# Optimization experiments

Hardware: AMD Instinct MI355X
Metric: run time of the kernel (lower is better)

The kernel has to match this reference:

```python
import jax, jax.numpy as jnp
import numpy as np

N = 50000      # nodes
E = 600000     # edges
G = 512        # graphs in batch
F_IN = 128     # input node features
H = 128        # hidden size (both layers)
PH = 128       # pool/classifier hidden size


def setup_inputs() -> dict:
    key = jax.random.key(0)
    ks = jax.random.split(key, 12)
    def lin(k, fi, fo):
        return (jax.random.normal(k, (fi, fo), jnp.float32) / np.sqrt(fi)).astype(jnp.float32)
    return {
        "x": jax.random.normal(ks[0], (N, F_IN), jnp.float32),
        "edge_index": jax.random.randint(ks[1], (2, E), 0, N),
        "batch": jnp.sort(jax.random.randint(ks[2], (N,), 0, G)),
        "W1": lin(ks[3], F_IN, H), "b1": jnp.zeros((H,), jnp.float32),
        "ln1_g": jnp.ones((H,), jnp.float32), "ln1_b": jnp.zeros((H,), jnp.float32),
        "W2": lin(ks[4], H, H), "b2": jnp.zeros((H,), jnp.float32),
        "ln2_g": jnp.ones((H,), jnp.float32), "ln2_b": jnp.zeros((H,), jnp.float32),
        "gate_w1": lin(ks[5], H, PH), "gate_b1": jnp.zeros((PH,), jnp.float32),
        "gate_w2": lin(ks[6], PH, 1), "gate_b2": jnp.zeros((1,), jnp.float32),
        "cls_w1": lin(ks[7], H, PH), "cls_b1": jnp.zeros((PH,), jnp.float32),
        "cls_w2": lin(ks[8], PH, 2), "cls_b2": jnp.zeros((2,), jnp.float32),
    }


def _layer_norm(h, g, b):
    m = h.mean(-1, keepdims=True)
    v = ((h - m) ** 2).mean(-1, keepdims=True)
    return (h - m) * jax.lax.rsqrt(v + 1e-5) * g + b


def _gcn(x, src, dst, norm, W, b):
    # GCNConv: x' = D^{-1/2} (A+I) D^{-1/2} (x W) + b
    h = x @ W
    out = jax.ops.segment_sum(h[src] * norm[:, None], dst, num_segments=N)
    return out + b


def reference(x, edge_index, batch, W1, b1, ln1_g, ln1_b, W2, b2, ln2_g, ln2_b,
              gate_w1, gate_b1, gate_w2, gate_b2, cls_w1, cls_b1, cls_w2, cls_b2):
    loops = jnp.arange(N, dtype=edge_index.dtype)
    src = jnp.concatenate([edge_index[0], loops])
    dst = jnp.concatenate([edge_index[1], loops])
    deg = jax.ops.segment_sum(jnp.ones_like(src, dtype=x.dtype), dst, num_segments=N)
    dinv = jnp.where(deg > 0, jax.lax.rsqrt(jnp.maximum(deg, 1e-12)), 0.0)
    norm = dinv[src] * dinv[dst]  # [(E+N)]

    h = jax.nn.relu(_layer_norm(_gcn(x, src, dst, norm, W1, b1), ln1_g, ln1_b))
    h = jax.nn.relu(_layer_norm(_gcn(h, src, dst, norm, W2, b2), ln2_g, ln2_b))

    # GlobalAttention pooling: gate MLP -> scatter softmax over graphs -> weighted sum
    gate = (jax.nn.relu(h @ gate_w1 + gate_b1) @ gate_w2 + gate_b2)[:, 0]  # [N]
    gmax = jax.ops.segment_max(gate, batch, num_segments=G)
    a = jnp.exp(gate - gmax[batch])
    denom = jax.ops.segment_sum(a, batch, num_segments=G)
    alpha = a / denom[batch]
    pooled = jax.ops.segment_sum(alpha[:, None] * h, batch, num_segments=G)  # [G, H]

    logits = jax.nn.relu(pooled @ cls_w1 + cls_b1) @ cls_w2 + cls_b2  # [G, 2]
    return logits
```

## Files before the change

kernel.cpp:

```cpp
#include <hip/hip_runtime.h>
#include <hip/hip_bf16.h>

typedef short s8v __attribute__((ext_vector_type(8)));
typedef float f4v __attribute__((ext_vector_type(4)));

__device__ __forceinline__ unsigned short f2bf(float f) {
  unsigned int u = __builtin_bit_cast(unsigned int, f);
  unsigned int r = u + 0x7fffu + ((u >> 16) & 1u);
  return (unsigned short)(r >> 16);
}
__device__ __forceinline__ float bf2f(unsigned short s) {
  return __builtin_bit_cast(float, ((unsigned int)s) << 16);
}
__device__ __forceinline__ float bflo(unsigned int v) {
  return __builtin_bit_cast(float, (unsigned int)(v << 16));
}
__device__ __forceinline__ float bfhi(unsigned int v) {
  return __builtin_bit_cast(float, (unsigned int)(v & 0xffff0000u));
}
__device__ __forceinline__ unsigned int packbf(float a, float b) {
  return (unsigned int)f2bf(a) | ((unsigned int)f2bf(b) << 16);
}

__device__ __forceinline__ int lower_bound_i(const int* a, int n, int key) {
  int lo = 0, hi = n;
  while (lo < hi) { int mid = (lo + hi) >> 1; if (a[mid] < key) lo = mid + 1; else hi = mid; }
  return lo;
}

__global__ void accum_deg(const int* __restrict__ dst, unsigned int* __restrict__ deg, int E) {
  int e = blockIdx.x * blockDim.x + threadIdx.x;
  if (e < E) atomicAdd(&deg[dst[e]], 1u);
}

__global__ __launch_bounds__(256) void scanA(const unsigned int* __restrict__ deg,
                                             int* __restrict__ offs, int* __restrict__ partial,
                                             float* __restrict__ dinv, int n) {
  __shared__ int sh[256];
  int t = threadIdx.x;
  int i = blockIdx.x * 256 + t;
  int v = (i < n) ? (int)deg[i] : 0;
  if (i < n) dinv[i] = rsqrtf((float)(deg[i] + 1u));
  sh[t] = v;
  __syncthreads();
  for (int o = 1; o < 256; o <<= 1) {
    int add = (t >= o) ? sh[t - o] : 0;
    __syncthreads();
    sh[t] += add;
    __syncthreads();
  }
  if (i < n) offs[i] = sh[t] - v;
  if (t == 255) partial[blockIdx.x] = sh[255];
}

__global__ __launch_bounds__(256) void scanC(int* __restrict__ offs, const int* __restrict__ partial,
                                             int* __restrict__ cursor, int n, int E) {
  __shared__ int red[256];
  int bid = blockIdx.x;
  int t = threadIdx.x;
  int s = 0;
  for (int j = t; j < bid; j += 256) s += partial[j];
  red[t] = s;
  __syncthreads();
#pragma unroll
  for (int o = 128; o > 0; o >>= 1) {
    if (t < o) red[t] += red[t + o];
    __syncthreads();
  }
  int pre = red[0];
  int i = bid * 256 + t;
  if (i < n) {
    int o = offs[i] + pre;
    offs[i] = o;
    cursor[i] = o;
  }
  if (i == 0) offs[n] = E;
}

__global__ __launch_bounds__(256) void scatter_csr(const int* __restrict__ src, const int* __restrict__ dst,
                                                   int* __restrict__ cursor, int* __restrict__ col, int E) {
  int e = blockIdx.x * 256 + threadIdx.x;
  if (e < E) {
    int slot = atomicAdd(&cursor[dst[e]], 1);
    col[slot] = src[e];
  }
}

__global__ __launch_bounds__(256) void pack_w3(const float* __restrict__ Wa, const float* __restrict__ Wb,
                                               const float* __restrict__ Wc, unsigned short* __restrict__ P) {
  int gidx = blockIdx.x * 256 + threadIdx.x;
  if (gidx >= 3 * 32768) return;
  int which = gidx >> 15;
  int idx = gidx & 32767;
  const float* W = (which == 0) ? Wa : (which == 1) ? Wb : Wc;
  int j = idx & 15;
  int lane = (idx >> 4) & 63;
  int t = (idx >> 10) & 7;
  int c = (idx >> 13) & 3;
  int k = c * 32 + (lane >> 4) * 8 + (j & 7);
  int n = t * 16 + (lane & 15);
  float f = W[k * 128 + n];
  unsigned short hi = f2bf(f);
  unsigned short outv = (j < 8) ? hi : f2bf(f - bf2f(hi));
  P[gidx] = outv;
}

__global__ __launch_bounds__(256) void gemm_f32in(
    const float* __restrict__ in, const unsigned short* __restrict__ P,
    unsigned short* __restrict__ out, int n) {
  __shared__ unsigned short wlds[32768];
  int tid = threadIdx.x;
  for (int i = tid; i < 4096; i += 256)
    reinterpret_cast<uint4*>(wlds)[i] = reinterpret_cast<const uint4*>(P)[i];
  __syncthreads();

  int wave = tid >> 6, lane = tid & 63;
  int quad = lane >> 4, col = lane & 15;
  int base = blockIdx.x * 64 + wave * 16;
  int m = base + col;

  f4v acc[8];
#pragma unroll
  for (int t = 0; t < 8; ++t) acc[t] = (f4v){0.f, 0.f, 0.f, 0.f};

  for (int c = 0; c < 4; ++c) {
    s8v ah, al;
    float v[8];
    if (m < n) {
      const float4* xp = reinterpret_cast<const float4*>(in + (size_t)m * 128 + c * 32 + quad * 8);
      float4 v0 = xp[0], v1 = xp[1];
      v[0] = v0.x; v[1] = v0.y; v[2] = v0.z; v[3] = v0.w;
      v[4] = v1.x; v[5] = v1.y; v[6] = v1.z; v[7] = v1.w;
    } else {
#pragma unroll
      for (int j = 0; j < 8; ++j) v[j] = 0.f;
    }
#pragma unroll
    for (int j = 0; j < 8; ++j) {
      unsigned short h = f2bf(v[j]);
      ah[j] = (short)h;
      al[j] = (short)f2bf(v[j] - bf2f(h));
    }
#pragma unroll
    for (int t = 0; t < 8; ++t) {
      const s8v* bp = reinterpret_cast<const s8v*>(&wlds[((c * 8 + t) * 64 + lane) * 16]);
      s8v bh = bp[0], bl = bp[1];
      acc[t] = __builtin_amdgcn_mfma_f32_16x16x32_bf16(ah, bh, acc[t], 0, 0, 0);
      acc[t] = __builtin_amdgcn_mfma_f32_16x16x32_bf16(ah, bl, acc[t], 0, 0, 0);
      acc[t] = __builtin_amdgcn_mfma_f32_16x16x32_bf16(al, bh, acc[t], 0, 0, 0);
    }
  }
#pragma unroll
  for (int t = 0; t < 8; ++t)
#pragma unroll
    for (int r = 0; r < 4; ++r) {
      int mm = base + quad * 4 + r;
      if (mm < n) out[(size_t)mm * 128 + t * 16 + col] = f2bf(acc[t][r]);
    }
}

__global__ __launch_bounds__(256) void gemm_b16in(
    const unsigned short* __restrict__ in, const unsigned short* __restrict__ P,
    unsigned short* __restrict__ out, int n) {
  __shared__ unsigned short wlds[32768];
  int tid = threadIdx.x;
  for (int i = tid; i < 4096; i += 256)
    reinterpret_cast<uint4*>(wlds)[i] = reinterpret_cast<const uint4*>(P)[i];
  __syncthreads();

  int wave = tid >> 6, lane = tid & 63;
  int quad = lane >> 4, col = lane & 15;
  int base = blockIdx.x * 64 + wave * 16;
  int m = base + col;

  f4v acc[8];
#pragma unroll
  for (int t = 0; t < 8; ++t) acc[t] = (f4v){0.f, 0.f, 0.f, 0.f};

  for (int c = 0; c < 4; ++c) {
    s8v ah;
    if (m < n)
      ah = *reinterpret_cast<const s8v*>(in + (size_t)m * 128 + c * 32 + quad * 8);
    else
      ah = (s8v){0, 0, 0, 0, 0, 0, 0, 0};
#pragma unroll
    for (int t = 0; t < 8; ++t) {
      const s8v* bp = reinterpret_cast<const s8v*>(&wlds[((c * 8 + t) * 64 + lane) * 16]);
      s8v bh = bp[0], bl = bp[1];
      acc[t] = __builtin_amdgcn_mfma_f32_16x16x32_bf16(ah, bh, acc[t], 0, 0, 0);
      acc[t] = __builtin_amdgcn_mfma_f32_16x16x32_bf16(ah, bl, acc[t], 0, 0, 0);
    }
  }
#pragma unroll
  for (int t = 0; t < 8; ++t)
#pragma unroll
    for (int r = 0; r < 4; ++r) {
      int mm = base + quad * 4 + r;
      if (mm < n) out[(size_t)mm * 128 + t * 16 + col] = f2bf(acc[t][r]);
    }
}

__global__ __launch_bounds__(256) void gemm_gate(
    const unsigned short* __restrict__ in, const unsigned short* __restrict__ P,
    const float* __restrict__ gb1, const float* __restrict__ gw2,
    const float* __restrict__ gb2, float* __restrict__ gate, int n) {
  __shared__ unsigned short wlds[32768];
  int tid = threadIdx.x;
  for (int i = tid; i < 4096; i += 256)
    reinterpret_cast<uint4*>(wlds)[i] = reinterpret_cast<const uint4*>(P)[i];
  __syncthreads();

  int wave = tid >> 6, lane = tid & 63;
  int quad = lane >> 4, col = lane & 15;
  int base = blockIdx.x * 64 + wave * 16;
  int m = base + col;

  f4v acc[8];
#pragma unroll
  for (int t = 0; t < 8; ++t) acc[t] = (f4v){0.f, 0.f, 0.f, 0.f};

  for (int c = 0; c < 4; ++c) {
    s8v ah;
    if (m < n)
      ah = *reinterpret_cast<const s8v*>(in + (size_t)m * 128 + c * 32 + quad * 8);
    else
      ah = (s8v){0, 0, 0, 0, 0, 0, 0, 0};
#pragma unroll
    for (int t = 0; t < 8; ++t) {
      const s8v* bp = reinterpret_cast<const s8v*>(&wlds[((c * 8 + t) * 64 + lane) * 16]);
      s8v bh = bp[0], bl = bp[1];
      acc[t] = __builtin_amdgcn_mfma_f32_16x16x32_bf16(ah, bh, acc[t], 0, 0, 0);
      acc[t] = __builtin_amdgcn_mfma_f32_16x16x32_bf16(ah, bl, acc[t], 0, 0, 0);
    }
  }
  float bv[8], g2[8];
#pragma unroll
  for (int t = 0; t < 8; ++t) {
    bv[t] = gb1[t * 16 + col];
    g2[t] = gw2[t * 16 + col];
  }
  float gb2v = gb2[0];
#pragma unroll
  for (int r = 0; r < 4; ++r) {
    float p = 0.f;
#pragma unroll
    for (int t = 0; t < 8; ++t)
      p += fmaxf(acc[t][r] + bv[t], 0.f) * g2[t];
#pragma unroll
    for (int o = 1; o < 16; o <<= 1) p += __shfl_xor(p, o);
    int mm = base + quad * 4 + r;
    if (col == 0 && mm < n) gate[mm] = p + gb2v;
  }
}

__global__ __launch_bounds__(256) void gather_ln(
    const int* __restrict__ offs, const int* __restrict__ col,
    const float* __restrict__ dinv, const unsigned short* __restrict__ h,
    const float* __restrict__ bias, const float* __restrict__ gam,
    const float* __restrict__ bet, unsigned short* __restrict__ out, int n) {
  int wid = (int)((blockIdx.x * 256u + threadIdx.x) >> 6);
  int lane = threadIdx.x & 63;
  int grp = lane >> 4;
  int sub = lane & 15;
  int i = wid * 4 + grp;
  if (i >= n) return;
  const uint4* hu = reinterpret_cast<const uint4*>(h);
  float di = dinv[i];
  float sl = di * di;
  uint4 hv = hu[(size_t)i * 16 + sub];
  float4 b0v = reinterpret_cast<const float4*>(bias)[sub * 2];
  float4 b1v = reinterpret_cast<const float4*>(bias)[sub * 2 + 1];
  float v[8];
  v[0] = bflo(hv.x) * sl + b0v.x; v[1] = bfhi(hv.x) * sl + b0v.y;
  v[2] = bflo(hv.y) * sl + b0v.z; v[3] = bfhi(hv.y) * sl + b0v.w;
  v[4] = bflo(hv.z) * sl + b1v.x; v[5] = bfhi(hv.z) * sl + b1v.y;
  v[6] = bflo(hv.w) * sl + b1v.z; v[7] = bfhi(hv.w) * sl + b1v.w;
  int b0 = offs[i], b1 = offs[i + 1];
  int e = b0;
  for (; e + 4 <= b1; e += 4) {
    int s0 = col[e], s1 = col[e + 1], s2 = col[e + 2], s3 = col[e + 3];
    uint4 h0 = hu[(size_t)s0 * 16 + sub];
    uint4 h1 = hu[(size_t)s1 * 16 + sub];
    uint4 h2 = hu[(size_t)s2 * 16 + sub];
    uint4 h3 = hu[(size_t)s3 * 16 + sub];
    float n0 = dinv[s0] * di, n1 = dinv[s1] * di, n2 = dinv[s2] * di, n3 = dinv[s3] * di;
    v[0] += bflo(h0.x) * n0 + bflo(h1.x) * n1 + bflo(h2.x) * n2 + bflo(h3.x) * n3;
    v[1] += bfhi(h0.x) * n0 + bfhi(h1.x) * n1 + bfhi(h2.x) * n2 + bfhi(h3.x) * n3;
    v[2] += bflo(h0.y) * n0 + bflo(h1.y) * n1 + bflo(h2.y) * n2 + bflo(h3.y) * n3;
    v[3] += bfhi(h0.y) * n0 + bfhi(h1.y) * n1 + bfhi(h2.y) * n2 + bfhi(h3.y) * n3;
    v[4] += bflo(h0.z) * n0 + bflo(h1.z) * n1 + bflo(h2.z) * n2 + bflo(h3.z) * n3;
    v[5] += bfhi(h0.z) * n0 + bfhi(h1.z) * n1 + bfhi(h2.z) * n2 + bfhi(h3.z) * n3;
    v[6] += bflo(h0.w) * n0 + bflo(h1.w) * n1 + bflo(h2.w) * n2 + bflo(h3.w) * n3;
    v[7] += bfhi(h0.w) * n0 + bfhi(h1.w) * n1 + bfhi(h2.w) * n2 + bfhi(h3.w) * n3;
  }
  for (; e + 2 <= b1; e += 2) {
    int s0 = col[e], s1 = col[e + 1];
    uint4 h0 = hu[(size_t)s0 * 16 + sub];
    uint4 h1 = hu[(size_t)s1 * 16 + sub];
    float n0 = dinv[s0] * di, n1 = dinv[s1] * di;
    v[0] += bflo(h0.x) * n0 + bflo(h1.x) * n1;
    v[1] += bfhi(h0.x) * n0 + bfhi(h1.x) * n1;
    v[2] += bflo(h0.y) * n0 + bflo(h1.y) * n1;
    v[3] += bfhi(h0.y) * n0 + bfhi(h1.y) * n1;
    v[4] += bflo(h0.z) * n0 + bflo(h1.z) * n1;
    v[5] += bfhi(h0.z) * n0 + bfhi(h1.z) * n1;
    v[6] += bflo(h0.w) * n0 + bflo(h1.w) * n1;
    v[7] += bfhi(h0.w) * n0 + bfhi(h1.w) * n1;
  }
  if (e < b1) {
    int s0 = col[e];
    uint4 h0 = hu[(size_t)s0 * 16 + sub];
    float n0 = dinv[s0] * di;
    v[0] += bflo(h0.x) * n0; v[1] += bfhi(h0.x) * n0;
    v[2] += bflo(h0.y) * n0; v[3] += bfhi(h0.y) * n0;
    v[4] += bflo(h0.z) * n0; v[5] += bfhi(h0.z) * n0;
    v[6] += bflo(h0.w) * n0; v[7] += bfhi(h0.w) * n0;
  }
  float s = 0.f, q = 0.f;
#pragma unroll
  for (int j = 0; j < 8; ++j) { s += v[j]; q += v[j] * v[j]; }
#pragma unroll
  for (int o = 1; o < 16; o <<= 1) {
    s += __shfl_xor(s, o);
    q += __shfl_xor(q, o);
  }
  float m = s * (1.0f / 128.0f);
  float var = q * (1.0f / 128.0f) - m * m;
  float rs = rsqrtf(var + 1e-5f);
  float4 g0 = reinterpret_cast<const float4*>(gam)[sub * 2];
  float4 g1 = reinterpret_cast<const float4*>(gam)[sub * 2 + 1];
  float4 e0 = reinterpret_cast<const float4*>(bet)[sub * 2];
  float4 e1 = reinterpret_cast<const float4*>(bet)[sub * 2 + 1];
  uint4 ov;
  ov.x = packbf(fmaxf((v[0] - m) * rs * g0.x + e0.x, 0.f), fmaxf((v[1] - m) * rs * g0.y + e0.y, 0.f));
  ov.y = packbf(fmaxf((v[2] - m) * rs * g0.z + e0.z, 0.f), fmaxf((v[3] - m) * rs * g0.w + e0.w, 0.f));
  ov.z = packbf(fmaxf((v[4] - m) * rs * g1.x + e1.x, 0.f), fmaxf((v[5] - m) * rs * g1.y + e1.y, 0.f));
  ov.w = packbf(fmaxf((v[6] - m) * rs * g1.z + e1.z, 0.f), fmaxf((v[7] - m) * rs * g1.w + e1.w, 0.f));
  reinterpret_cast<uint4*>(out)[(size_t)i * 16 + sub] = ov;
}

__global__ __launch_bounds__(256) void pool_kernel(
    float* __restrict__ gate, const unsigned short* __restrict__ h,
    const int* __restrict__ batch, float* __restrict__ pooled, int n) {
  int g = blockIdx.x;
  int tid = threadIdx.x;
  __shared__ float red[256];
  __shared__ float red2[256];
  int lo = lower_bound_i(batch, n, g);
  int hi = lower_bound_i(batch, n, g + 1);
  if (lo >= hi) {
    if (tid < 128) pooled[(size_t)g * 128 + tid] = 0.0f;
    return;
  }
  float m = -3.0e38f;
  for (int i = lo + tid; i < hi; i += 256) m = fmaxf(m, gate[i]);
  red[tid] = m;
  __syncthreads();
#pragma unroll
  for (int o = 128; o > 0; o >>= 1) {
    if (tid < o) red[tid] = fmaxf(red[tid], red[tid + o]);
    __syncthreads();
  }
  m = red[0];
  __syncthreads();
  float s = 0.0f;
  for (int i = lo + tid; i < hi; i += 256) {
    float e = __expf(gate[i] - m);
    gate[i] = e;
    s += e;
  }
  red[tid] = s;
  __syncthreads();
#pragma unroll
  for (int o = 128; o > 0; o >>= 1) {
    if (tid < o) red[tid] += red[tid + o];
    __syncthreads();
  }
  float inv = 1.0f / red[0];
  __syncthreads();
  const unsigned int* hu = reinterpret_cast<const unsigned int*>(h);
  int j = tid & 63, rgp = tid >> 6;
  float a0 = 0.f, a1 = 0.f;
  int i = lo + rgp;
  for (; i + 4 < hi; i += 8) {
    unsigned int p0 = hu[(size_t)i * 64 + j];
    unsigned int p1 = hu[(size_t)(i + 4) * 64 + j];
    float w0 = gate[i], w1 = gate[i + 4];
    a0 += bflo(p0) * w0 + bflo(p1) * w1;
    a1 += bfhi(p0) * w0 + bfhi(p1) * w1;
  }
  if (i < hi) {
    unsigned int p0 = hu[(size_t)i * 64 + j];
    float w0 = gate[i];
    a0 += bflo(p0) * w0;
    a1 += bfhi(p0) * w0;
  }
  red[tid] = a0;
  red2[tid] = a1;
  __syncthreads();
  if (tid < 64) {
    float f0 = (red[tid] + red[tid + 64] + red[tid + 128] + red[tid + 192]) * inv;
    float f1 = (red2[tid] + red2[tid + 64] + red2[tid + 128] + red2[tid + 192]) * inv;
    reinterpret_cast<float2*>(pooled + (size_t)g * 128)[tid] = make_float2(f0, f1);
  }
}

__global__ __launch_bounds__(128) void classifier(
    const float* __restrict__ pooled, const float* __restrict__ w1,
    const float* __restrict__ b1, const float* __restrict__ w2,
    const float* __restrict__ b2, float* __restrict__ out) {
  int g = blockIdx.x, j = threadIdx.x;
  __shared__ float p[128];
  __shared__ float r[128];
  p[j] = pooled[(size_t)g * 128 + j];
  __syncthreads();
  float acc = 0.0f;
#pragma unroll 8
  for (int k = 0; k < 128; ++k) acc = fmaf(p[k], w1[k * 128 + j], acc);
  acc += b1[j];
  r[j] = fmaxf(acc, 0.0f);
  __syncthreads();
  if (j < 2) {
    float a = 0.0f;
    for (int k = 0; k < 128; ++k) a = fmaf(r[k], w2[k * 2 + j], a);
    out[g * 2 + j] = a + b2[j];
  }
}

static inline size_t alup(size_t x) { return (x + 255) & ~(size_t)255; }

extern "C" void kernel_launch(void* const* d_in, const int* in_sizes, int n_in,
                              void* d_out, int out_size, void* d_ws, size_t ws_size,
                              hipStream_t stream) {
  const float* x    = (const float*)d_in[0];
  const int*   ei   = (const int*)d_in[1];
  const int*   bat  = (const int*)d_in[2];
  const float* W1   = (const float*)d_in[3];
  const float* b1   = (const float*)d_in[4];
  const float* ln1g = (const float*)d_in[5];
  const float* ln1b = (const float*)d_in[6];
  const float* W2   = (const float*)d_in[7];
  const float* b2   = (const float*)d_in[8];
  const float* ln2g = (const float*)d_in[9];
  const float* ln2b = (const float*)d_in[10];
  const float* gw1  = (const float*)d_in[11];
  const float* gb1  = (const float*)d_in[12];
  const float* gw2  = (const float*)d_in[13];
  const float* gb2  = (const float*)d_in[14];
  const float* cw1  = (const float*)d_in[15];
  const float* cb1  = (const float*)d_in[16];
  const float* cw2  = (const float*)d_in[17];
  const float* cb2  = (const float*)d_in[18];

  const int N = in_sizes[2];
  const int E = in_sizes[1] / 2;
  const int G = out_size / 2;
  const int* src = ei;
  const int* dst = ei + E;

  int nb256 = (N + 255) / 256;
  int eb256 = (E + 255) / 256;
  int mfmaB = (N + 63) / 64;
  int gatherB = (N + 15) / 16;

  char* base = (char*)d_ws;
  unsigned int* deg = (unsigned int*)base; base += alup((size_t)N * 4);
  float* dinv = (float*)base;              base += alup((size_t)N * 4);
  int* offs = (int*)base;                  base += alup((size_t)(N + 1) * 4);
  int* cursor = (int*)base;                base += alup((size_t)N * 4);
  int* partial = (int*)base;               base += alup((size_t)nb256 * 4);
  int* col = (int*)base;                   base += alup((size_t)E * 4);
  unsigned short* pW = (unsigned short*)base; base += alup((size_t)3 * 32768 * 2);
  unsigned short* hbuf = (unsigned short*)base; base += alup((size_t)N * 128 * 2);
  unsigned short* hout = (unsigned short*)base; base += alup((size_t)N * 128 * 2);
  float* gate = (float*)base;              base += alup((size_t)N * 4);
  float* pooled = (float*)base;            base += alup((size_t)G * 128 * 4);

  unsigned short* pW1 = pW;
  unsigned short* pW2 = pW + 32768;
  unsigned short* pG1 = pW + 65536;

  float* out = (float*)d_out;

  hipMemsetAsync(deg, 0, (size_t)N * 4, stream);
  accum_deg<<<eb256, 256, 0, stream>>>(dst, deg, E);
  scanA<<<nb256, 256, 0, stream>>>(deg, offs, partial, dinv, N);
  scanC<<<nb256, 256, 0, stream>>>(offs, partial, cursor, N, E);
  scatter_csr<<<eb256, 256, 0, stream>>>(src, dst, cursor, col, E);
  pack_w3<<<384, 256, 0, stream>>>(W1, W2, gw1, pW);

  gemm_f32in<<<mfmaB, 256, 0, stream>>>(x, pW1, hbuf, N);
  gather_ln<<<gatherB, 256, 0, stream>>>(offs, col, dinv, hbuf, b1, ln1g, ln1b, hout, N);

  gemm_b16in<<<mfmaB, 256, 0, stream>>>(hout, pW2, hbuf, N);
  gather_ln<<<gatherB, 256, 0, stream>>>(offs, col, dinv, hbuf, b2, ln2g, ln2b, hout, N);

  gemm_gate<<<mfmaB, 256, 0, stream>>>(hout, pG1, gb1, gw2, gb2, gate, N);

  pool_kernel<<<G, 256, 0, stream>>>(gate, hout, bat, pooled, N);

  classifier<<<G, 128, 0, stream>>>(pooled, cw1, cb1, cw2, cb2, out);
}
```

Before: 289.7 us.

## Fuse launches: pack+zero, gemm1+CSR scatter, pool+classifier; store dinv with edge indices

Several small kernels are merged to cut launch count. The weight packing and degree zeroing become one kernel. The CSR scatter runs as extra blocks of the first GEMM launch. Pooling and the classifier become one kernel, which removes the pooled buffer. The CSR column array now stores each source's dinv next to its index, so the gather avoids a dependent dinv load, at the cost of twice the column-array bandwidth. The scatter and GEMM blocks in one grid also contend for occupancy, since every block reserves the 64KB LDS even when it only scatters.

```diff
diff --git a/kernel.cpp b/kernel.cpp
--- a/kernel.cpp
+++ b/kernel.cpp
@@ -26,6 +26,31 @@
   int lo = 0, hi = n;
   while (lo < hi) { int mid = (lo + hi) >> 1; if (a[mid] < key) lo = mid + 1; else hi = mid; }
   return lo;
+}
+
+__global__ __launch_bounds__(256) void pack_zero(
+    const float* __restrict__ Wa, const float* __restrict__ Wb, const float* __restrict__ Wc,
+    unsigned short* __restrict__ P, unsigned int* __restrict__ deg, int n) {
+  int bid = blockIdx.x;
+  if (bid >= 384) {
+    int i = (bid - 384) * 256 + threadIdx.x;
+    if (i < n) deg[i] = 0u;
+    return;
+  }
+  int gidx = bid * 256 + threadIdx.x;
+  int which = gidx >> 15;
+  int idx = gidx & 32767;
+  const float* W = (which == 0) ? Wa : (which == 1) ? Wb : Wc;
+  int j = idx & 15;
+  int lane = (idx >> 4) & 63;
+  int t = (idx >> 10) & 7;
+  int c = (idx >> 13) & 3;
+  int k = c * 32 + (lane >> 4) * 8 + (j & 7);
+  int nn = t * 16 + (lane & 15);
+  float f = W[k * 128 + nn];
+  unsigned short hi = f2bf(f);
+  unsigned short outv = (j < 8) ? hi : f2bf(f - bf2f(hi));
+  P[gidx] = outv;
 }
 
 __global__ void accum_deg(const int* __restrict__ dst, unsigned int* __restrict__ deg, int E) {
@@ -77,38 +102,23 @@
   if (i == 0) offs[n] = E;
 }
 
-__global__ __launch_bounds__(256) void scatter_csr(const int* __restrict__ src, const int* __restrict__ dst,
-                                                   int* __restrict__ cursor, int* __restrict__ col, int E) {
-  int e = blockIdx.x * 256 + threadIdx.x;
-  if (e < E) {
-    int slot = atomicAdd(&cursor[dst[e]], 1);
-    col[slot] = src[e];
-  }
-}
-
-__global__ __launch_bounds__(256) void pack_w3(const float* __restrict__ Wa, const float* __restrict__ Wb,
-                                               const float* __restrict__ Wc, unsigned short* __restrict__ P) {
-  int gidx = blockIdx.x * 256 + threadIdx.x;
-  if (gidx >= 3 * 32768) return;
-  int which = gidx >> 15;
-  int idx = gidx & 32767;
-  const float* W = (which == 0) ? Wa : (which == 1) ? Wb : Wc;
-  int j = idx & 15;
-  int lane = (idx >> 4) & 63;
-  int t = (idx >> 10) & 7;
-  int c = (idx >> 13) & 3;
-  int k = c * 32 + (lane >> 4) * 8 + (j & 7);
-  int n = t * 16 + (lane & 15);
-  float f = W[k * 128 + n];
-  unsigned short hi = f2bf(f);
-  unsigned short outv = (j < 8) ? hi : f2bf(f - bf2f(hi));
-  P[gidx] = outv;
-}
-
-__global__ __launch_bounds__(256) void gemm_f32in(
+__global__ __launch_bounds__(256) void gemm1_scatter(
     const float* __restrict__ in, const unsigned short* __restrict__ P,
-    unsigned short* __restrict__ out, int n) {
+    unsigned short* __restrict__ out, int n,
+    const int* __restrict__ src, const int* __restrict__ dst,
+    int* __restrict__ cursor, int2* __restrict__ col2,
+    const float* __restrict__ dinv, int E, int gemmBlocks) {
   __shared__ unsigned short wlds[32768];
+  if ((int)blockIdx.x >= gemmBlocks) {
+    int e = ((int)blockIdx.x - gemmBlocks) * 256 + threadIdx.x;
+    if (e < E) {
+      int d = dst[e];
+      int s = src[e];
+      int slot = atomicAdd(&cursor[d], 1);
+      col2[slot] = make_int2(s, __builtin_bit_cast(int, dinv[s]));
+    }
+    return;
+  }
   int tid = threadIdx.x;
   for (int i = tid; i < 4096; i += 256)
     reinterpret_cast<uint4*>(wlds)[i] = reinterpret_cast<const uint4*>(P)[i];
@@ -254,7 +264,7 @@
 }
 
 __global__ __launch_bounds__(256) void gather_ln(
-    const int* __restrict__ offs, const int* __restrict__ col,
+    const int* __restrict__ offs, const int2* __restrict__ col2,
     const float* __restrict__ dinv, const unsigned short* __restrict__ h,
     const float* __restrict__ bias, const float* __restrict__ gam,
     const float* __restrict__ bet, unsigned short* __restrict__ out, int n) {
@@ -278,12 +288,15 @@
   int b0 = offs[i], b1 = offs[i + 1];
   int e = b0;
   for (; e + 4 <= b1; e += 4) {
-    int s0 = col[e], s1 = col[e + 1], s2 = col[e + 2], s3 = col[e + 3];
-    uint4 h0 = hu[(size_t)s0 * 16 + sub];
-    uint4 h1 = hu[(size_t)s1 * 16 + sub];
-    uint4 h2 = hu[(size_t)s2 * 16 + sub];
-    uint4 h3 = hu[(size_t)s3 * 16 + sub];
-    float n0 = dinv[s0] * di, n1 = dinv[s1] * di, n2 = dinv[s2] * di, n3 = dinv[s3] * di;
+    int2 c0 = col2[e], c1 = col2[e + 1], c2 = col2[e + 2], c3 = col2[e + 3];
+    uint4 h0 = hu[(size_t)c0.x * 16 + sub];
+    uint4 h1 = hu[(size_t)c1.x * 16 + sub];
+    uint4 h2 = hu[(size_t)c2.x * 16 + sub];
+    uint4 h3 = hu[(size_t)c3.x * 16 + sub];
+    float n0 = __builtin_bit_cast(float, c0.y) * di;
+    float n1 = __builtin_bit_cast(float, c1.y) * di;
+    float n2 = __builtin_bit_cast(float, c2.y) * di;
+    float n3 = __builtin_bit_cast(float, c3.y) * di;
     v[0] += bflo(h0.x) * n0 + bflo(h1.x) * n1 + bflo(h2.x) * n2 + bflo(h3.x) * n3;
     v[1] += bfhi(h0.x) * n0 + bfhi(h1.x) * n1 + bfhi(h2.x) * n2 + bfhi(h3.x) * n3;
     v[2] += bflo(h0.y) * n0 + bflo(h1.y) * n1 + bflo(h2.y) * n2 + bflo(h3.y) * n3;
@@ -293,24 +306,10 @@
     v[6] += bflo(h0.w) * n0 + bflo(h1.w) * n1 + bflo(h2.w) * n2 + bflo(h3.w) * n3;
     v[7] += bfhi(h0.w) * n0 + bfhi(h1.w) * n1 + bfhi(h2.w) * n2 + bfhi(h3.w) * n3;
   }
-  for (; e + 2 <= b1; e += 2) {
-    int s0 = col[e], s1 = col[e + 1];
-    uint4 h0 = hu[(size_t)s0 * 16 + sub];
-    uint4 h1 = hu[(size_t)s1 * 16 + sub];
-    float n0 = dinv[s0] * di, n1 = dinv[s1] * di;
-    v[0] += bflo(h0.x) * n0 + bflo(h1.x) * n1;
-    v[1] += bfhi(h0.x) * n0 + bfhi(h1.x) * n1;
-    v[2] += bflo(h0.y) * n0 + bflo(h1.y) * n1;
-    v[3] += bfhi(h0.y) * n0 + bfhi(h1.y) * n1;
-    v[4] += bflo(h0.z) * n0 + bflo(h1.z) * n1;
-    v[5] += bfhi(h0.z) * n0 + bfhi(h1.z) * n1;
-    v[6] += bflo(h0.w) * n0 + bflo(h1.w) * n1;
-    v[7] += bfhi(h0.w) * n0 + bfhi(h1.w) * n1;
-  }
-  if (e < b1) {
-    int s0 = col[e];
-    uint4 h0 = hu[(size_t)s0 * 16 + sub];
-    float n0 = dinv[s0] * di;
+  for (; e < b1; ++e) {
+    int2 c0 = col2[e];
+    uint4 h0 = hu[(size_t)c0.x * 16 + sub];
+    float n0 = __builtin_bit_cast(float, c0.y) * di;
     v[0] += bflo(h0.x) * n0; v[1] += bfhi(h0.x) * n0;
     v[2] += bflo(h0.y) * n0; v[3] += bfhi(h0.y) * n0;
     v[4] += bflo(h0.z) * n0; v[5] += bfhi(h0.z) * n0;
@@ -339,91 +338,88 @@
   reinterpret_cast<uint4*>(out)[(size_t)i * 16 + sub] = ov;
 }
 
-__global__ __launch_bounds__(256) void pool_kernel(
+__global__ __launch_bounds__(256) void pool_cls(
     float* __restrict__ gate, const unsigned short* __restrict__ h,
-    const int* __restrict__ batch, float* __restrict__ pooled, int n) {
+    const int* __restrict__ batch,
+    const float* __restrict__ w1, const float* __restrict__ b1,
+    const float* __restrict__ w2, const float* __restrict__ b2,
+    float* __restrict__ out, int n) {
   int g = blockIdx.x;
   int tid = threadIdx.x;
   __shared__ float red[256];
   __shared__ float red2[256];
+  __shared__ float p[128];
+  __shared__ float r[128];
   int lo = lower_bound_i(batch, n, g);
   int hi = lower_bound_i(batch, n, g + 1);
   if (lo >= hi) {
-    if (tid < 128) pooled[(size_t)g * 128 + tid] = 0.0f;
-    return;
-  }
-  float m = -3.0e38f;
-  for (int i = lo + tid; i < hi; i += 256) m = fmaxf(m, gate[i]);
-  red[tid] = m;
-  __syncthreads();
-#pragma unroll
-  for (int o = 128; o > 0; o >>= 1) {
-    if (tid < o) red[tid] = fmaxf(red[tid], red[tid + o]);
-    __syncthreads();
-  }
-  m = red[0];
-  __syncthreads();
-  float s = 0.0f;
-  for (int i = lo + tid; i < hi; i += 256) {
-    float e = __expf(gate[i] - m);
-    gate[i] = e;
-    s += e;
-  }
-  red[tid] = s;
-  __syncthreads();
-#pragma unroll
-  for (int o = 128; o > 0; o >>= 1) {
-    if (tid < o) red[tid] += red[tid + o];
-    __syncthreads();
-  }
-  float inv = 1.0f / red[0];
-  __syncthreads();
-  const unsigned int* hu = reinterpret_cast<const unsigned int*>(h);
-  int j = tid & 63, rgp = tid >> 6;
-  float a0 = 0.f, a1 = 0.f;
-  int i = lo + rgp;
-  for (; i + 4 < hi; i += 8) {
-    unsigned int p0 = hu[(size_t)i * 64 + j];
-    unsigned int p1 = hu[(size_t)(i + 4) * 64 + j];
-    float w0 = gate[i], w1 = gate[i + 4];
-    a0 += bflo(p0) * w0 + bflo(p1) * w1;
-    a1 += bfhi(p0) * w0 + bfhi(p1) * w1;
-  }
-  if (i < hi) {
-    unsigned int p0 = hu[(size_t)i * 64 + j];
-    float w0 = gate[i];
-    a0 += bflo(p0) * w0;
-    a1 += bfhi(p0) * w0;
-  }
-  red[tid] = a0;
-  red2[tid] = a1;
-  __syncthreads();
-  if (tid < 64) {
-    float f0 = (red[tid] + red[tid + 64] + red[tid + 128] + red[tid + 192]) * inv;
-    float f1 = (red2[tid] + red2[tid + 64] + red2[tid + 128] + red2[tid + 192]) * inv;
-    reinterpret_cast<float2*>(pooled + (size_t)g * 128)[tid] = make_float2(f0, f1);
-  }
-}
-
-__global__ __launch_bounds__(128) void classifier(
-    const float* __restrict__ pooled, const float* __restrict__ w1,
-    const float* __restrict__ b1, const float* __restrict__ w2,
-    const float* __restrict__ b2, float* __restrict__ out) {
-  int g = blockIdx.x, j = threadIdx.x;
-  __shared__ float p[128];
-  __shared__ float r[128];
-  p[j] = pooled[(size_t)g * 128 + j];
-  __syncthreads();
+    if (tid < 128) p[tid] = 0.0f;
+  } else {
+    float m = -3.0e38f;
+    for (int i = lo + tid; i < hi; i += 256) m = fmaxf(m, gate[i]);
+    red[tid] = m;
+    __syncthreads();
+#pragma unroll
+    for (int o = 128; o > 0; o >>= 1) {
+      if (tid < o) red[tid] = fmaxf(red[tid], red[tid + o]);
+      __syncthreads();
+    }
+    m = red[0];
+    __syncthreads();
+    float s = 0.0f;
+    for (int i = lo + tid; i < hi; i += 256) {
+      float e = __expf(gate[i] - m);
+      gate[i] = e;
+      s += e;
+    }
+    red[tid] = s;
+    __syncthreads();
+#pragma unroll
+    for (int o = 128; o > 0; o >>= 1) {
+      if (tid < o) red[tid] += red[tid + o];
+      __syncthreads();
+    }
+    float inv = 1.0f / red[0];
+    __syncthreads();
+    const unsigned int* hu = reinterpret_cast<const unsigned int*>(h);
+    int j = tid & 63, rgp = tid >> 6;
+    float a0 = 0.f, a1 = 0.f;
+    int i = lo + rgp;
+    for (; i + 4 < hi; i += 8) {
+      unsigned int p0 = hu[(size_t)i * 64 + j];
+      unsigned int p1 = hu[(size_t)(i + 4) * 64 + j];
+      float w0 = gate[i], w1v = gate[i + 4];
+      a0 += bflo(p0) * w0 + bflo(p1) * w1v;
+      a1 += bfhi(p0) * w0 + bfhi(p1) * w1v;
+    }
+    if (i < hi) {
+      unsigned int p0 = hu[(size_t)i * 64 + j];
+      float w0 = gate[i];
+      a0 += bflo(p0) * w0;
+      a1 += bfhi(p0) * w0;
+    }
+    red[tid] = a0;
+    red2[tid] = a1;
+    __syncthreads();
+    if (tid < 64) {
+      p[2 * tid]     = (red[tid] + red[tid + 64] + red[tid + 128] + red[tid + 192]) * inv;
+      p[2 * tid + 1] = (red2[tid] + red2[tid + 64] + red2[tid + 128] + red2[tid + 192]) * inv;
+    }
+  }
+  __syncthreads();
+  int j = tid & 127, half = tid >> 7;
   float acc = 0.0f;
 #pragma unroll 8
-  for (int k = 0; k < 128; ++k) acc = fmaf(p[k], w1[k * 128 + j], acc);
-  acc += b1[j];
-  r[j] = fmaxf(acc, 0.0f);
-  __syncthreads();
-  if (j < 2) {
+  for (int k = half * 64; k < half * 64 + 64; ++k)
+    acc = fmaf(p[k], w1[k * 128 + j], acc);
+  red[tid] = acc;
+  __syncthreads();
+  if (tid < 128) r[tid] = fmaxf(red[tid] + red[tid + 128] + b1[tid], 0.0f);
+  __syncthreads();
+  if (tid < 2) {
     float a = 0.0f;
-    for (int k = 0; k < 128; ++k) a = fmaf(r[k], w2[k * 2 + j], a);
-    out[g * 2 + j] = a + b2[j];
+    for (int k = 0; k < 128; ++k) a = fmaf(r[k], w2[k * 2 + tid], a);
+    out[g * 2 + tid] = a + b2[tid];
   }
 }
 
@@ -469,12 +465,11 @@
   int* offs = (int*)base;                  base += alup((size_t)(N + 1) * 4);
   int* cursor = (int*)base;                base += alup((size_t)N * 4);
   int* partial = (int*)base;               base += alup((size_t)nb256 * 4);
-  int* col = (int*)base;                   base += alup((size_t)E * 4);
+  int2* col2 = (int2*)base;                base += alup((size_t)E * 8);
   unsigned short* pW = (unsigned short*)base; base += alup((size_t)3 * 32768 * 2);
   unsigned short* hbuf = (unsigned short*)base; base += alup((size_t)N * 128 * 2);
   unsigned short* hout = (unsigned short*)base; base += alup((size_t)N * 128 * 2);
   float* gate = (float*)base;              base += alup((size_t)N * 4);
-  float* pooled = (float*)base;            base += alup((size_t)G * 128 * 4);
 
   unsigned short* pW1 = pW;
   unsigned short* pW2 = pW + 32768;
@@ -482,22 +477,15 @@
 
   float* out = (float*)d_out;
 
-  hipMemsetAsync(deg, 0, (size_t)N * 4, stream);
+  pack_zero<<<384 + nb256, 256, 0, stream>>>(W1, W2, gw1, pW, deg, N);
   accum_deg<<<eb256, 256, 0, stream>>>(dst, deg, E);
   scanA<<<nb256, 256, 0, stream>>>(deg, offs, partial, dinv, N);
   scanC<<<nb256, 256, 0, stream>>>(offs, partial, cursor, N, E);
-  scatter_csr<<<eb256, 256, 0, stream>>>(src, dst, cursor, col, E);
-  pack_w3<<<384, 256, 0, stream>>>(W1, W2, gw1, pW);
-
-  gemm_f32in<<<mfmaB, 256, 0, stream>>>(x, pW1, hbuf, N);
-  gather_ln<<<gatherB, 256, 0, stream>>>(offs, col, dinv, hbuf, b1, ln1g, ln1b, hout, N);
-
+  gemm1_scatter<<<mfmaB + eb256, 256, 0, stream>>>(x, pW1, hbuf, N,
+                                                   src, dst, cursor, col2, dinv, E, mfmaB);
+  gather_ln<<<gatherB, 256, 0, stream>>>(offs, col2, dinv, hbuf, b1, ln1g, ln1b, hout, N);
   gemm_b16in<<<mfmaB, 256, 0, stream>>>(hout, pW2, hbuf, N);
-  gather_ln<<<gatherB, 256, 0, stream>>>(offs, col, dinv, hbuf, b2, ln2g, ln2b, hout, N);
-
+  gather_ln<<<gatherB, 256, 0, stream>>>(offs, col2, dinv, hbuf, b2, ln2g, ln2b, hout, N);
   gemm_gate<<<mfmaB, 256, 0, stream>>>(hout, pG1, gb1, gw2, gb2, gate, N);
-
-  pool_kernel<<<G, 256, 0, stream>>>(gate, hout, bat, pooled, N);
-
-  classifier<<<G, 128, 0, stream>>>(pooled, cw1, cb1, cw2, cb2, out);
-}
+  pool_cls<<<G, 256, 0, stream>>>(gate, hout, bat, cw1, cb1, cw2, cb2, out, N);
+}
```

New measurement: 281.5 us. -2.8%, faster.
